# Kernel tuning notes

Hardware: AMD Instinct MI355X
Metric: run time of the kernel (lower is better)

Reference implementation:

```python
import jax, jax.numpy as jnp
import numpy as np

# ---- static dims ----
B, L, V = 8, 512, 100000
E, NERD, COREFD = 100, 20, 20          # word / ner / coref embedding dims
H, DIS, REL, HT = 128, 20, 97, 512     # hidden, dis embed, relations, n_pairs
W, N, R, C = 512, 32, 8, 256           # DNC word len, cells, read heads, ctrl hidden
IN_SIZE = E + NERD + COREFD            # 140 == H + 12 (required by final_layer)
DNC_OUT = H + 12                        # 140
CTRL_IN = IN_SIZE + R * W               # 4236
MASK_MIN, EPS, CLIP = 0.1, 1e-6, 20.0
# interface vector layout: read keys, read strengths, write key, write strength,
# erase, write vec, free gates, alloc gate, write gate, read modes,
# write mask, read masks, fwd sharpness, bwd sharpness
XI_SIZES = [R*W, R, W, 1, W, W, R, 1, 1, 3*R, W, R*W, R, R]
XI = sum(XI_SIZES)


def setup_inputs():
    key = jax.random.key(0)
    ks = iter(jax.random.split(key, 40))
    def nrm(shape, s=0.02):
        return (jax.random.normal(next(ks), shape) * s).astype(jnp.float32)
    def ri(shape, hi):
        return jax.random.randint(next(ks), shape, 0, hi)
    return dict(
        context_idxs=ri((B, L), V),
        pos=ri((B, L), L),
        context_ner=ri((B, L), 7),
        context_char_idxs=ri((B, L, 16), 262),
        context_lens=jnp.full((B,), L, dtype=jnp.int32),
        h_mapping=jax.random.uniform(next(ks), (B, HT, L), jnp.float32) / L,
        t_mapping=jax.random.uniform(next(ks), (B, HT, L), jnp.float32) / L,
        relation_mask=jnp.ones((B, HT), jnp.float32),
        dis_h_2_t=ri((B, HT), 20),
        dis_t_2_h=ri((B, HT), 20),
        word_emb=nrm((V, E), 0.1),
        entity_emb=nrm((L, COREFD), 0.1),
        ner_emb=nrm((7, NERD), 0.1),
        dis_emb=nrm((20, DIS), 0.1),
        Wih0=nrm((CTRL_IN, 4*C)), Whh0=nrm((C, 4*C)), b0=jnp.zeros((4*C,), jnp.float32),
        Wih1=nrm((C, 4*C)), Whh1=nrm((C, 4*C)), b1=jnp.zeros((4*C,), jnp.float32),
        Wih2=nrm((C, 4*C)), Whh2=nrm((C, 4*C)), b2=jnp.zeros((4*C,), jnp.float32),
        W_xi=nrm((C, XI)), b_xi=jnp.zeros((XI,), jnp.float32),
        W_out=nrm((C + R*W, DNC_OUT)), b_out=jnp.zeros((DNC_OUT,), jnp.float32),
        W_final=nrm((DNC_OUT, 2*H)), b_final=jnp.zeros((2*H,), jnp.float32),
        W_re=nrm((2*H, H)), b_re=jnp.zeros((H,), jnp.float32),
        W_bili=nrm((REL, H+DIS, H+DIS)), b_bili=jnp.zeros((REL,), jnp.float32),
    )


def _lstm(x, h, c, Wih, Whh, b):
    z = x @ Wih + h @ Whh + b
    i, f, g, o = jnp.split(z, 4, axis=-1)
    c = jax.nn.sigmoid(f) * c + jax.nn.sigmoid(i) * jnp.tanh(g)
    h = jax.nn.sigmoid(o) * jnp.tanh(c)
    return h, c


def _content(M, key_, beta, mask):
    # M [B,N,W]; key_, mask [B,h,W]; beta [B,h] -> weights [B,h,N]
    k = key_ * mask
    Mm = M[:, None] * mask[:, :, None]                 # [B,h,N,W]
    dot = jnp.einsum('bhw,bhnw->bhn', k, Mm)
    kn = jnp.linalg.norm(k, axis=-1)[..., None]
    Mn = jnp.linalg.norm(Mm, axis=-1)
    cos = dot / (kn * Mn + EPS)
    return jax.nn.softmax(beta[..., None] * cos, axis=-1)


def _sharpen(w, s):
    w = (w + EPS) ** s[..., None]
    return w / w.sum(-1, keepdims=True)


def _dnc(x, params):
    (Wih0, Whh0, b0, Wih1, Whh1, b1, Wih2, Whh2, b2, W_xi, b_xi, W_out, b_out) = params
    Bs = x.shape[0]
    eye = jnp.eye(N, dtype=x.dtype)
    splits = np.cumsum(XI_SIZES)[:-1]

    def step(carry, x_t):
        (h0, c0, h1, c1, h2, c2, M, u, wr, ww, p, Lnk, reads) = carry
        ci = jnp.concatenate([x_t, reads.reshape(Bs, R*W)], -1)
        h0, c0 = _lstm(ci, h0, c0, Wih0, Whh0, b0)
        h1, c1 = _lstm(h0, h1, c1, Wih1, Whh1, b1)
        h2, c2 = _lstm(h1, h2, c2, Wih2, Whh2, b2)
        h = jnp.clip(h2, -CLIP, CLIP)
        xi = h @ W_xi + b_xi
        (rk, rb, wk, wb, er, wv, fg, ga, gw, rm,
         wmask, rmask, sf, sb) = jnp.split(xi, splits, axis=-1)
        rk = rk.reshape(Bs, R, W)
        rb = 1 + jax.nn.softplus(rb)                    # [B,R]
        wk = wk.reshape(Bs, 1, W)
        wb = 1 + jax.nn.softplus(wb)                    # [B,1]
        er = jax.nn.sigmoid(er)                         # [B,W]
        fg = jax.nn.sigmoid(fg)                         # [B,R]
        ga = jax.nn.sigmoid(ga)
        gw = jax.nn.sigmoid(gw)
        pi = jax.nn.softmax(rm.reshape(Bs, R, 3), -1)
        wmask = MASK_MIN + (1 - MASK_MIN) * jax.nn.sigmoid(wmask)
        rmask = MASK_MIN + (1 - MASK_MIN) * jax.nn.sigmoid(rmask).reshape(Bs, R, W)
        sf = 1 + jax.nn.softplus(sf)
        sb = 1 + jax.nn.softplus(sb)

        # retention / usage
        psi = jnp.prod(1 - fg[:, :, None] * wr, axis=1)  # [B,N]
        u = (u + ww - u * ww) * psi
        # allocation weighting via sorted free list
        order = jnp.argsort(u, axis=-1)
        us = jnp.take_along_axis(u, order, -1)
        cp = jnp.cumprod(jnp.concatenate([jnp.ones((Bs, 1), u.dtype), us[:, :-1]], -1), -1)
        a_s = (1 - us) * cp
        a = jnp.zeros_like(u).at[jnp.arange(Bs)[:, None], order].set(a_s)
        # write addressing (masked content + allocation)
        cw = _content(M, wk, wb, wmask[:, None, :])[:, 0]
        ww = gw * (ga * a + (1 - ga) * cw)
        # de-allocate content of freed cells, then write
        M = M * psi[:, :, None]
        M = M * (1 - ww[:, :, None] * er[:, None, :]) + ww[:, :, None] * wv[:, None, :]
        # temporal link matrix (uses previous precedence p)
        Lnk = (1 - ww[:, :, None] - ww[:, None, :]) * Lnk + ww[:, :, None] * p[:, None, :]
        Lnk = Lnk * (1 - eye)
        p = (1 - ww.sum(-1, keepdims=True)) * p + ww
        # read addressing with link sharpness control
        fw = _sharpen(jnp.einsum('bij,brj->bri', Lnk, wr), sf)
        bw = _sharpen(jnp.einsum('bji,brj->bri', Lnk, wr), sb)
        cr = _content(M, rk, rb, rmask)
        wr = pi[..., 0:1] * bw + pi[..., 1:2] * cr + pi[..., 2:3] * fw
        reads = jnp.einsum('brn,bnw->brw', wr, M)
        y = jnp.concatenate([h, reads.reshape(Bs, R*W)], -1) @ W_out + b_out
        return (h0, c0, h1, c1, h2, c2, M, u, wr, ww, p, Lnk, reads), y

    z = jnp.zeros
    carry0 = (z((Bs, C)), z((Bs, C)), z((Bs, C)), z((Bs, C)), z((Bs, C)), z((Bs, C)),
              z((Bs, N, W)), z((Bs, N)), z((Bs, R, N)), z((Bs, N)), z((Bs, N)),
              z((Bs, N, N)), z((Bs, R, W)))
    _, ys = jax.lax.scan(step, carry0, x.transpose(1, 0, 2))
    return ys.transpose(1, 0, 2)  # [B,L,DNC_OUT]


def reference(context_idxs, pos, context_ner, context_char_idxs, context_lens,
              h_mapping, t_mapping, relation_mask, dis_h_2_t, dis_t_2_h,
              word_emb, entity_emb, ner_emb, dis_emb,
              Wih0, Whh0, b0, Wih1, Whh1, b1, Wih2, Whh2, b2,
              W_xi, b_xi, W_out, b_out, W_final, b_final, W_re, b_re,
              W_bili, b_bili):
    sent = jnp.concatenate([word_emb[context_idxs], entity_emb[pos],
                            ner_emb[context_ner]], -1)      # [B,L,140]
    dnc_params = (Wih0, Whh0, b0, Wih1, Whh1, b1, Wih2, Whh2, b2,
                  W_xi, b_xi, W_out, b_out)
    out = _dnc(sent, dnc_params)                             # [B,L,140]
    out = out @ W_final + b_final                            # LockedDropout: identity (eval)
    ctx = jax.nn.relu(out @ W_re + b_re)                     # [B,L,H]
    s0 = jnp.einsum('bpl,blh->bph', h_mapping, ctx)
    t0 = jnp.einsum('bpl,blh->bph', t_mapping, ctx)
    s_rep = jnp.concatenate([s0, dis_emb[dis_h_2_t]], -1)    # [B,P,148]
    t_rep = jnp.concatenate([t0, dis_emb[dis_t_2_h]], -1)
    return jnp.einsum('bpi,kij,bpj->bpk', s_rep, W_bili, t_rep) + b_bili
```

## Files before the change

### kernel.cpp

```cpp
#include <hip/hip_runtime.h>
#include <math.h>

#define B8      8
#define LSEQ    512
#define NWG     256
#define TPB     512
#define RELK    97
#define BI      148
#define FSTR    16
#define LDSF    39040
#define LDSB    (LDSF*4)

__device__ __forceinline__ float sigf(float x){
  return (x >= 0.f) ? 1.f/(1.f + expf(-x)) : expf(x)/(1.f + expf(x));
}
__device__ __forceinline__ float spf(float x){
  return (x > 0.f) ? x + log1pf(expf(-x)) : log1pf(expf(x));
}

__device__ __forceinline__ float agld(const float* p){
  return __hip_atomic_load(p, __ATOMIC_RELAXED, __HIP_MEMORY_SCOPE_AGENT);
}
__device__ __forceinline__ void agst(float* p, float v){
  __hip_atomic_store(p, v, __ATOMIC_RELAXED, __HIP_MEMORY_SCOPE_AGENT);
}

__global__ __launch_bounds__(256)
void k_sent(const int* __restrict__ cidx, const int* __restrict__ pos,
            const int* __restrict__ ner, const float* __restrict__ wemb,
            const float* __restrict__ eemb, const float* __restrict__ nemb,
            float* __restrict__ sent)
{
  int flat = blockIdx.x*256 + threadIdx.x;
  if (flat >= B8*LSEQ*140) return;
  int d = flat % 140; int bl = flat / 140;
  float v;
  if (d < 100)      v = wemb[(size_t)cidx[bl]*100 + d];
  else if (d < 120) v = eemb[(size_t)pos[bl]*20 + (d-100)];
  else              v = nemb[(size_t)ner[bl]*20 + (d-120)];
  sent[flat] = v;
}

__global__ __launch_bounds__(256)
void k_tr(const float* __restrict__ A, const float* __restrict__ Bsrc,
          int N, int K1a, int K1b, int K2, long long total, float* __restrict__ T)
{
  long long i = (long long)blockIdx.x*256 + threadIdx.x;
  if (i >= total) return;
  int k = (int)(i % K2);
  long long c = i / K2;
  float v = 0.f;
  if (k < K1a)            v = A[(size_t)k*N + c];
  else if (k < K1a+K1b)   v = Bsrc[(size_t)(k-K1a)*N + c];
  T[i] = v;
}

__device__ __forceinline__ void gbar(int* flags, int* genrep, int seq){
  __syncthreads();
  const int tid = threadIdx.x;
  const int bid = blockIdx.x;
  if (tid == 0){
    asm volatile("s_waitcnt vmcnt(0)" ::: "memory");
    __hip_atomic_store(&flags[bid*FSTR], seq, __ATOMIC_RELAXED, __HIP_MEMORY_SCOPE_AGENT);
  }
  if (bid == 0){
    if (tid < NWG){
      while (__hip_atomic_load(&flags[tid*FSTR], __ATOMIC_RELAXED, __HIP_MEMORY_SCOPE_AGENT) < seq)
        __builtin_amdgcn_s_sleep(2);
    }
    __syncthreads();
    if (tid < 32)
      __hip_atomic_store(&genrep[tid*FSTR], seq, __ATOMIC_RELAXED, __HIP_MEMORY_SCOPE_AGENT);
  } else if (tid == 0){
    while (__hip_atomic_load(&genrep[(bid & 31)*FSTR], __ATOMIC_RELAXED, __HIP_MEMORY_SCOPE_AGENT) < seq)
      __builtin_amdgcn_s_sleep(2);
  }
  __syncthreads();
}

__device__ void mem_phase(float* lds, const float* __restrict__ xi,
                          float* __restrict__ M, float* u_g, float* ww_g,
                          float* p_g, float* wr_g, float* L_g, float* rout)
{
  const int tid = threadIdx.x;
  float* mL  = lds;
  float* mwr = lds+1024;
  float* mwrn= lds+1280;
  float* mcr = lds+1536;
  float* mfw = lds+1792;
  float* mbw = lds+2048;
  float* PSI = lds+2304;
  float* UU  = lds+2336;
  float* US  = lds+2368;
  float* AA  = lds+2400;
  float* CW  = lds+2432;
  float* WWN = lds+2464;
  float* WWO = lds+2496;
  float* PP  = lds+2528;
  int*   mord= (int*)(lds+2560);
  float* mh  = lds+2592;
  float* mpi = lds+2656;
  float* msc = lds+2688;
  float* q1  = lds+2752;
  float* q2  = lds+3264;

  if (tid < 8){
    mh[tid]    = 1.f + spf(agld(&xi[4096+tid]));
    mh[8+tid]  = 1.f + spf(agld(&xi[10283+tid]));
    mh[16+tid] = 1.f + spf(agld(&xi[10291+tid]));
    mh[24+tid] = sigf(agld(&xi[5641+tid]));
    float e0=agld(&xi[5651+3*tid]), e1=agld(&xi[5652+3*tid]), e2=agld(&xi[5653+3*tid]);
    float mx=fmaxf(e0,fmaxf(e1,e2));
    float x0=expf(e0-mx), x1=expf(e1-mx), x2=expf(e2-mx);
    float inv=1.f/(x0+x1+x2);
    mpi[tid*3]=x0*inv; mpi[tid*3+1]=x1*inv; mpi[tid*3+2]=x2*inv;
  }
  if (tid==0){ msc[0]=1.f+spf(agld(&xi[4616])); msc[1]=sigf(agld(&xi[5649])); msc[2]=sigf(agld(&xi[5650])); }
  if (tid<32){ UU[tid]=u_g[tid]; WWO[tid]=ww_g[tid]; PP[tid]=p_g[tid]; }
  if (tid<256) mwr[tid]=wr_g[tid];
  mL[tid]=L_g[tid]; mL[tid+512]=L_g[tid+512];
  { float wm = 0.1f+0.9f*sigf(agld(&xi[5675+tid])); q1[tid]=agld(&xi[4104+tid])*wm; q2[tid]=wm; }
  __syncthreads();

  if (tid<32){
    float psi=1.f;
    #pragma unroll
    for (int r=0;r<8;r++) psi *= (1.f - mh[24+r]*mwr[r*32+tid]);
    PSI[tid]=psi;
    float uo=UU[tid], wo=WWO[tid];
    UU[tid]=(uo+wo-uo*wo)*psi;
  }
  __syncthreads();
  if (tid<32){
    float un=UU[tid]; int rank=0;
    for (int m=0;m<32;m++){ float um=UU[m]; rank += (um<un)||(um==un && m<tid); }
    mord[rank]=tid;
  }
  __syncthreads();
  if (tid<32) US[tid]=UU[mord[tid]];
  __syncthreads();
  if (tid==0){ float cp=1.f; for (int j=0;j<32;j++){ AA[mord[j]]=(1.f-US[j])*cp; cp*=US[j]; } }
  __syncthreads();

  { float q=q1[tid]*q1[tid];
    for (int o=32;o;o>>=1) q += __shfl_down(q,o,64);
    if ((tid&63)==0) msc[8+(tid>>6)]=q; }
  __syncthreads();
  if (tid==0){ float q=0.f; for (int i=0;i<8;i++) q+=msc[8+i]; msc[3]=sqrtf(q); }
  __syncthreads();
  { int n=tid>>4, wsub=tid&15;
    float d=0.f,q=0.f;
    for (int i=0;i<32;i++){ int w=wsub+16*i; float m=M[(size_t)n*512+w]; float t2=m*q2[w]; d+=q1[w]*t2; q+=t2*t2; }
    for (int o=8;o;o>>=1){ d+=__shfl_down(d,o,16); q+=__shfl_down(q,o,16); }
    if (wsub==0){ float cs=d/(msc[3]*sqrtf(q)+1e-6f); CW[n]=msc[0]*cs; } }
  __syncthreads();
  if (tid==0){ float mx=-1e30f; for(int n=0;n<32;n++) mx=fmaxf(mx,CW[n]); msc[4]=mx; }
  __syncthreads();
  if (tid<32) CW[tid]=expf(CW[tid]-msc[4]);
  __syncthreads();
  if (tid==0){ float sm=0.f; for(int n=0;n<32;n++) sm+=CW[n]; msc[5]=1.f/sm; }
  __syncthreads();
  if (tid<32) CW[tid]*=msc[5];
  __syncthreads();
  if (tid<32) WWN[tid]=msc[2]*(msc[1]*AA[tid]+(1.f-msc[1])*CW[tid]);
  __syncthreads();
  { float er=sigf(agld(&xi[4617+tid])); float wv=agld(&xi[5129+tid]);
    for (int n=0;n<32;n++){ size_t idx=(size_t)n*512+tid; float m=M[idx];
      M[idx]=m*PSI[n]*(1.f-WWN[n]*er)+WWN[n]*wv; } }
  __syncthreads();
  for (int ii=0;ii<2;ii++){ int f=tid+512*ii; int i=f>>5, j=f&31;
    float nl=(1.f-WWN[i]-WWN[j])*mL[f]+WWN[i]*PP[j];
    mL[f]=(i==j)?0.f:nl; }
  __syncthreads();
  if (tid==0){ float sw=0.f; for(int n=0;n<32;n++) sw+=WWN[n]; msc[6]=sw; }
  __syncthreads();
  if (tid<32) PP[tid]=(1.f-msc[6])*PP[tid]+WWN[tid];
  __syncthreads();
  { int r=(tid>>5)&7, i=tid&31; bool isB=(tid>=256);
    float accv=0.f;
    if (!isB){ for (int j=0;j<32;j++) accv += mL[i*32+j]*mwr[r*32+j]; }
    else     { for (int j=0;j<32;j++) accv += mL[j*32+i]*mwr[r*32+j]; }
    float sp = isB? mh[16+r] : mh[8+r];
    float e = expf(sp*logf(accv+1e-6f));
    if (!isB) mfw[r*32+i]=e; else mbw[r*32+i]=e; }
  __syncthreads();
  if (tid<16){ int r=tid&7; float sm=0.f;
    if (tid<8){ for(int n=0;n<32;n++) sm+=mfw[r*32+n]; msc[16+r]=1.f/sm; }
    else      { for(int n=0;n<32;n++) sm+=mbw[r*32+n]; msc[24+r]=1.f/sm; } }
  __syncthreads();
  { int r=(tid>>5)&7, i=tid&31; bool isB=(tid>=256);
    if (!isB) mfw[r*32+i]*=msc[16+r]; else mbw[r*32+i]*=msc[24+r]; }
  __syncthreads();
  for (int r=0;r<8;r++){
    { float rm=0.1f+0.9f*sigf(agld(&xi[6187+r*512+tid]));
      q1[tid]=agld(&xi[r*512+tid])*rm; q2[tid]=rm; }
    __syncthreads();
    { float q=q1[tid]*q1[tid];
      for (int o=32;o;o>>=1) q+=__shfl_down(q,o,64);
      if ((tid&63)==0) msc[8+(tid>>6)]=q; }
    __syncthreads();
    if (tid==0){ float qq=0.f; for(int i=0;i<8;i++) qq+=msc[8+i]; msc[32]=sqrtf(qq); }
    __syncthreads();
    { int n=tid>>4, wsub=tid&15;
      float d=0.f,q=0.f;
      for (int i=0;i<32;i++){ int w=wsub+16*i; float m=M[(size_t)n*512+w]; float t2=m*q2[w]; d+=q1[w]*t2; q+=t2*t2; }
      for (int o=8;o;o>>=1){ d+=__shfl_down(d,o,16); q+=__shfl_down(q,o,16); }
      if (wsub==0){ float cs=d/(msc[32]*sqrtf(q)+1e-6f); mcr[r*32+n]=mh[r]*cs; } }
    __syncthreads();
  }
  if (tid<8){ int r=tid; float mx=-1e30f;
    for (int n=0;n<32;n++) mx=fmaxf(mx,mcr[r*32+n]);
    float sm=0.f;
    for (int n=0;n<32;n++){ float e=expf(mcr[r*32+n]-mx); mcr[r*32+n]=e; sm+=e; }
    float inv=1.f/sm;
    for (int n=0;n<32;n++) mcr[r*32+n]*=inv; }
  __syncthreads();
  if (tid<256){ int r=tid>>5, n=tid&31;
    float v=mpi[r*3]*mbw[r*32+n]+mpi[r*3+1]*mcr[r*32+n]+mpi[r*3+2]*mfw[r*32+n];
    mwrn[tid]=v; wr_g[tid]=v; }
  __syncthreads();
  { int r=tid>>6, wsub=tid&63;
    for (int i2=0;i2<8;i2++){ int w=wsub+64*i2;
      float accv=0.f;
      for (int n=0;n<32;n++) accv+=mwrn[r*32+n]*M[(size_t)n*512+w];
      agst(&rout[r*512+w], accv); } }
  if (tid<32){ u_g[tid]=UU[tid]; ww_g[tid]=WWN[tid]; p_g[tid]=PP[tid]; }
  L_g[tid]=mL[tid]; L_g[tid+512]=mL[tid+512];
}

__global__ __launch_bounds__(TPB, 1)
void dnc_persist(
  const float* __restrict__ sent,
  const float* __restrict__ WAg, const float* __restrict__ b0,
  const float* __restrict__ W1g, const float* __restrict__ b1,
  const float* __restrict__ W2g, const float* __restrict__ b2,
  const float* __restrict__ WXIg,const float* __restrict__ bxi,
  const float* __restrict__ WY,  const float* __restrict__ bout,
  float* __restrict__ Hh, float* __restrict__ yh,
  float* __restrict__ reads2,
  float* __restrict__ h0g, float* __restrict__ h1g, float* __restrict__ h2g,
  float* __restrict__ c0g, float* __restrict__ c1g, float* __restrict__ c2g,
  float* __restrict__ z0g, float* __restrict__ z1g, float* __restrict__ z2g,
  float* __restrict__ xig,
  float* __restrict__ Mb, float* __restrict__ ug, float* __restrict__ wwg,
  float* __restrict__ pg, float* __restrict__ wrg, float* __restrict__ Lg,
  int* flags, int* genrep)
{
  extern __shared__ float lds[];
  float* sA   = lds;
  float* sRed = lds + 4160;
  float* wA   = lds + 4224;
  float* w1l  = lds + 22656;
  float* w2l  = lds + 24704;
  float* wxl  = lds + 26752;
  const int wg  = blockIdx.x;
  const int tid = threadIdx.x;
  const int cq = tid >> 7, kq = tid & 127;
  const int xc = tid >> 6, xk = tid & 63;
  int seq = 0;

  for (int f=tid; f<18432; f+=TPB) wA[f]  = WAg[(size_t)wg*18432 + f];
  for (int f=tid; f<2048;  f+=TPB) w1l[f] = W1g[(size_t)wg*2048  + f];
  for (int f=tid; f<2048;  f+=TPB) w2l[f] = W2g[(size_t)wg*2048  + f];
  for (int f=tid; f<12288; f+=TPB){
    int cl = f>>8, k = f&255; int col = wg*48 + cl;
    wxl[f] = (col < 10299) ? WXIg[(size_t)col*256 + k] : 0.f;
  }
  const bool isy = (wg >= 8 && wg < 148);
  const float* wcolY = WY + (size_t)(isy ? (wg-8) : 0)*4352;
  __syncthreads();

  #pragma unroll 1
  for (int t=0; t<LSEQ; t++){
    const int rp = t&1, wp = rp^1, pprev = (t+1)&1;
    const float* readsPrev = reads2 + (size_t)pprev*32768;

    {
      const float* h0p = h0g + pprev*2048;
      float acc[8] = {0,0,0,0,0,0,0,0};
      float av[8];
      #pragma unroll
      for (int s=0;s<8;s++){
        int kg = tid;
        av[s] = (kg<140) ? sent[((size_t)s*512 + t)*140 + kg]
                         : agld(&readsPrev[s*4096 + kg - 140]);
      }
      #pragma unroll 1
      for (int ch=0; ch<9; ch++){
        __syncthreads();
        #pragma unroll
        for (int s=0;s<8;s++) sA[s*520 + tid] = av[s];
        __syncthreads();
        if (ch < 8){
          int kg = (ch+1)*512 + tid;
          #pragma unroll
          for (int s=0;s<8;s++){
            float v;
            if (kg < 140)       v = sent[((size_t)s*512 + t)*140 + kg];
            else if (kg < 4236) v = agld(&readsPrev[s*4096 + kg - 140]);
            else if (kg < 4492) v = agld(&h0p[s*256 + (kg-4236)]);
            else                v = 0.f;
            av[s]=v;
          }
        }
        float4 wv = *reinterpret_cast<const float4*>(&wA[cq*4608 + ch*512 + (kq<<2)]);
        #pragma unroll
        for (int s=0;s<8;s++){
          float4 a = *reinterpret_cast<const float4*>(&sA[s*520 + (kq<<2)]);
          acc[s] += a.x*wv.x + a.y*wv.y + a.z*wv.z + a.w*wv.w;
        }
      }
      #pragma unroll
      for (int o=32;o;o>>=1)
        #pragma unroll
        for (int s=0;s<8;s++) acc[s]+=__shfl_down(acc[s],o,64);
      if ((tid&63)==0){ int wv2=tid>>6;
        #pragma unroll
        for (int s=0;s<8;s++) sRed[wv2*8+s]=acc[s]; }
      __syncthreads();
      if (tid<32){ int c=tid>>3, s=tid&7;
        agst(&z0g[s*1024 + wg*4 + c], sRed[c*16+s] + sRed[c*16+8+s] + b0[wg*4+c]); }
    }
    gbar(flags,genrep,++seq);

    {
      float4 w1v = *reinterpret_cast<const float4*>(&w1l[cq*512 + (kq<<2)]);
      if (tid<256){
        int j=tid;
        #pragma unroll
        for (int s=0;s<8;s++){
          float zi=agld(&z0g[s*1024+j]), zf=agld(&z0g[s*1024+256+j]);
          float zg=agld(&z0g[s*1024+512+j]), zo=agld(&z0g[s*1024+768+j]);
          float cold=agld(&c0g[rp*2048+s*256+j]);
          float cn=sigf(zf)*cold+sigf(zi)*tanhf(zg);
          float h=sigf(zo)*tanhf(cn);
          sA[s*520+j]=h;
          if (wg==8){ agst(&c0g[wp*2048+s*256+j],cn); agst(&h0g[rp*2048+s*256+j],h); }
        }
      } else {
        int j=tid-256;
        const float* h1p = h1g + pprev*2048;
        #pragma unroll
        for (int s=0;s<8;s++) sA[s*520+256+j]=agld(&h1p[s*256+j]);
      }
      __syncthreads();
      float acc[8]={0,0,0,0,0,0,0,0};
      #pragma unroll
      for (int s=0;s<8;s++){
        float4 a=*reinterpret_cast<const float4*>(&sA[s*520+(kq<<2)]);
        acc[s]+=a.x*w1v.x+a.y*w1v.y+a.z*w1v.z+a.w*w1v.w;
      }
      #pragma unroll
      for (int o=32;o;o>>=1)
        #pragma unroll
        for (int s=0;s<8;s++) acc[s]+=__shfl_down(acc[s],o,64);
      if ((tid&63)==0){ int wv2=tid>>6;
        #pragma unroll
        for (int s=0;s<8;s++) sRed[wv2*8+s]=acc[s]; }
      __syncthreads();
      if (tid<32){ int c=tid>>3, s=tid&7;
        agst(&z1g[s*1024 + wg*4 + c], sRed[c*16+s] + sRed[c*16+8+s] + b1[wg*4+c]); }
    }
    gbar(flags,genrep,++seq);

    {
      float4 w2v = *reinterpret_cast<const float4*>(&w2l[cq*512 + (kq<<2)]);
      if (tid<256){
        int j=tid;
        #pragma unroll
        for (int s=0;s<8;s++){
          float zi=agld(&z1g[s*1024+j]), zf=agld(&z1g[s*1024+256+j]);
          float zg=agld(&z1g[s*1024+512+j]), zo=agld(&z1g[s*1024+768+j]);
          float cold=agld(&c1g[rp*2048+s*256+j]);
          float cn=sigf(zf)*cold+sigf(zi)*tanhf(zg);
          float h=sigf(zo)*tanhf(cn);
          sA[s*520+j]=h;
          if (wg==8){ agst(&c1g[wp*2048+s*256+j],cn); agst(&h1g[rp*2048+s*256+j],h); }
        }
      } else {
        int j=tid-256;
        const float* h2p = h2g + pprev*2048;
        #pragma unroll
        for (int s=0;s<8;s++) sA[s*520+256+j]=agld(&h2p[s*256+j]);
      }
      __syncthreads();
      float acc[8]={0,0,0,0,0,0,0,0};
      #pragma unroll
      for (int s=0;s<8;s++){
        float4 a=*reinterpret_cast<const float4*>(&sA[s*520+(kq<<2)]);
        acc[s]+=a.x*w2v.x+a.y*w2v.y+a.z*w2v.z+a.w*w2v.w;
      }
      #pragma unroll
      for (int o=32;o;o>>=1)
        #pragma unroll
        for (int s=0;s<8;s++) acc[s]+=__shfl_down(acc[s],o,64);
      if ((tid&63)==0){ int wv2=tid>>6;
        #pragma unroll
        for (int s=0;s<8;s++) sRed[wv2*8+s]=acc[s]; }
      __syncthreads();
      if (tid<32){ int c=tid>>3, s=tid&7;
        agst(&z2g[s*1024 + wg*4 + c], sRed[c*16+s] + sRed[c*16+8+s] + b2[wg*4+c]); }
    }
    gbar(flags,genrep,++seq);

    {
      if (tid<256){
        int j=tid;
        #pragma unroll
        for (int s=0;s<8;s++){
          float zi=agld(&z2g[s*1024+j]), zf=agld(&z2g[s*1024+256+j]);
          float zg=agld(&z2g[s*1024+512+j]), zo=agld(&z2g[s*1024+768+j]);
          float cold=agld(&c2g[rp*2048+s*256+j]);
          float cn=sigf(zf)*cold+sigf(zi)*tanhf(zg);
          float h2=sigf(zo)*tanhf(cn);
          float hc=fminf(fmaxf(h2,-20.f),20.f);
          sA[s*520+j]=hc;
          if (wg==8){ agst(&c2g[wp*2048+s*256+j],cn); agst(&h2g[rp*2048+s*256+j],h2);
                      agst(&Hh[((size_t)t*8+s)*256+j],hc); }
        }
      }
      __syncthreads();
      float accx[6][8];
      #pragma unroll
      for (int cc=0;cc<6;cc++)
        #pragma unroll
        for (int s=0;s<8;s++) accx[cc][s]=0.f;
      #pragma unroll
      for (int s=0;s<8;s++){
        float4 a = *reinterpret_cast<const float4*>(&sA[s*520 + (xk<<2)]);
        #pragma unroll
        for (int cc=0;cc<6;cc++){
          float4 wv = *reinterpret_cast<const float4*>(&wxl[(xc*6+cc)*256 + (xk<<2)]);
          accx[cc][s] += a.x*wv.x + a.y*wv.y + a.z*wv.z + a.w*wv.w;
        }
      }
      #pragma unroll
      for (int o=32;o;o>>=1)
        #pragma unroll
        for (int cc=0;cc<6;cc++)
          #pragma unroll
          for (int s=0;s<8;s++) accx[cc][s]+=__shfl_down(accx[cc][s],o,64);
      if ((tid&63)==0){
        #pragma unroll
        for (int cc=0;cc<6;cc++){
          int col = wg*48 + xc*6 + cc;
          if (col < 10299){
            #pragma unroll
            for (int s=0;s<8;s++) agst(&xig[(size_t)s*10299+col], accx[cc][s]+bxi[col]);
          }
        }
      }
    }
    gbar(flags,genrep,++seq);

    if (wg < 8){
      mem_phase(lds, xig + (size_t)wg*10299, Mb + (size_t)wg*16384,
                ug+wg*32, wwg+wg*32, pg+wg*32, wrg+wg*256, Lg+wg*1024,
                reads2 + (size_t)rp*32768 + wg*4096);
    } else if (isy && t > 0){
      int ty = t-1;
      const float* rdp = reads2 + (size_t)(ty&1)*32768;
      float wy[9];
      #pragma unroll
      for (int ch=0;ch<9;ch++){ int k=ch*512+tid; wy[ch]=(k<4352)? wcolY[k] : 0.f; }
      float acy[8]={0,0,0,0,0,0,0,0};
      #pragma unroll
      for (int ch=0;ch<9;ch++){
        int kg=ch*512+tid;
        #pragma unroll
        for (int s=0;s<8;s++){
          float a;
          if (kg<256)       a=agld(&Hh[((size_t)ty*8+s)*256+kg]);
          else if (kg<4352) a=agld(&rdp[s*4096+kg-256]);
          else              a=0.f;
          acy[s]+=a*wy[ch];
        }
      }
      #pragma unroll
      for (int o=32;o;o>>=1)
        #pragma unroll
        for (int s=0;s<8;s++) acy[s]+=__shfl_down(acy[s],o,64);
      if ((tid&63)==0){ int wv2=tid>>6;
        #pragma unroll
        for (int s=0;s<8;s++) sRed[wv2*8+s]=acy[s]; }
      __syncthreads();
      if (tid<8){ float v=0.f;
        #pragma unroll
        for (int w=0;w<8;w++) v+=sRed[w*8+tid];
        yh[((size_t)tid*512+ty)*140+(wg-8)]=v+bout[wg-8]; }
    }
    gbar(flags,genrep,++seq);
  }

  if (isy){
    int ty = 511;
    const float* rdp = reads2 + (size_t)(ty&1)*32768;
    float wy[9];
    #pragma unroll
    for (int ch=0;ch<9;ch++){ int k=ch*512+tid; wy[ch]=(k<4352)? wcolY[k] : 0.f; }
    float acy[8]={0,0,0,0,0,0,0,0};
    #pragma unroll
    for (int ch=0;ch<9;ch++){
      int kg=ch*512+tid;
      #pragma unroll
      for (int s=0;s<8;s++){
        float a;
        if (kg<256)       a=agld(&Hh[((size_t)ty*8+s)*256+kg]);
        else if (kg<4352) a=agld(&rdp[s*4096+kg-256]);
        else              a=0.f;
        acy[s]+=a*wy[ch];
      }
    }
    #pragma unroll
    for (int o=32;o;o>>=1)
      #pragma unroll
      for (int s=0;s<8;s++) acy[s]+=__shfl_down(acy[s],o,64);
    if ((tid&63)==0){ int wv2=tid>>6;
      #pragma unroll
      for (int s=0;s<8;s++) sRed[wv2*8+s]=acy[s]; }
    __syncthreads();
    if (tid<8){ float v=0.f;
      #pragma unroll
      for (int w=0;w<8;w++) v+=sRed[w*8+tid];
      yh[((size_t)tid*512+ty)*140+(wg-8)]=v+bout[wg-8]; }
  }
}

__global__ __launch_bounds__(256)
void gemm16(int M, int N, int K,
            const float* __restrict__ A, long long sAb, int lda,
            const float* __restrict__ Bm, long long sBb, int ldb,
            float* __restrict__ C, long long sCb, int ldc,
            const float* __restrict__ bias, int relu)
{
  __shared__ float sAh[16*512];
  const int tid = threadIdx.x;
  const float* Ab = A + (size_t)blockIdx.y*sAb;
  const float* Bb = Bm + (size_t)blockIdx.y*sBb;
  float* Cb = C + (size_t)blockIdx.y*sCb;
  const int m0 = blockIdx.x*16;
  const int tot = 16*K;
  for (int f = tid; f < tot; f += 256) sAh[f] = Ab[(size_t)m0*lda + f];
  __syncthreads();
  int c = (tid & 63)*4; int rg = tid >> 6;
  if (c >= N) return;
  float acc[4][4] = {};
  for (int k=0;k<K;k++){
    float4 bv = *reinterpret_cast<const float4*>(Bb + (size_t)k*ldb + c);
    #pragma unroll
    for (int rr=0;rr<4;rr++){
      float a = sAh[(rg*4+rr)*K + k];
      acc[rr][0] += a*bv.x; acc[rr][1] += a*bv.y; acc[rr][2] += a*bv.z; acc[rr][3] += a*bv.w;
    }
  }
  for (int rr=0;rr<4;rr++){
    int m = m0 + rg*4 + rr;
    #pragma unroll
    for (int e=0;e<4;e++){
      float v = acc[rr][e] + (bias ? bias[c+e] : 0.f);
      if (relu) v = fmaxf(v, 0.f);
      Cb[(size_t)m*ldc + c + e] = v;
    }
  }
}

__global__ __launch_bounds__(256)
void bilin(const float* __restrict__ s0, const float* __restrict__ t0,
           const float* __restrict__ dis_emb, const int* __restrict__ dht,
           const int* __restrict__ dth, const float* __restrict__ Wb,
           const float* __restrict__ bb, float* __restrict__ out)
{
  __shared__ float sS[BI][33];
  __shared__ float sT[32][152];
  const int tid = threadIdx.x;
  const int bp0 = blockIdx.x*32;
  for (int f = tid; f < 32*BI; f += 256){
    int pp = f / BI, i = f % BI;
    int bp = bp0 + pp;
    float sv, tv;
    if (i < 128){ sv = s0[(size_t)bp*128 + i]; tv = t0[(size_t)bp*128 + i]; }
    else {
      sv = dis_emb[(size_t)dht[bp]*20 + (i-128)];
      tv = dis_emb[(size_t)dth[bp]*20 + (i-128)];
    }
    sS[i][pp] = sv; sT[pp][i] = tv;
  }
  __syncthreads();
  const int ppg = tid >> 5, jb = tid & 31;
  const int pp0 = ppg*4;
  const int k0 = blockIdx.y*49, kend = min(k0+49, RELK);
  for (int k = k0; k < kend; k++){
    const float* Wk = Wb + (size_t)k*BI*BI;
    float acc[4][5];
    #pragma unroll
    for (int a=0;a<4;a++) for (int b=0;b<5;b++) acc[a][b]=0.f;
    for (int i=0;i<BI;i++){
      float sv0 = sS[i][pp0], sv1 = sS[i][pp0+1], sv2 = sS[i][pp0+2], sv3 = sS[i][pp0+3];
      const float* wrow = Wk + i*BI;
      #pragma unroll
      for (int jj=0;jj<5;jj++){
        int j = jb + 32*jj;
        if (j < BI){
          float w = wrow[j];
          acc[0][jj] += sv0*w; acc[1][jj] += sv1*w; acc[2][jj] += sv2*w; acc[3][jj] += sv3*w;
        }
      }
    }
    float dot[4] = {0.f,0.f,0.f,0.f};
    #pragma unroll
    for (int jj=0;jj<5;jj++){
      int j = jb + 32*jj;
      if (j < BI){
        #pragma unroll
        for (int p4=0;p4<4;p4++) dot[p4] += acc[p4][jj]*sT[pp0+p4][j];
      }
    }
    #pragma unroll
    for (int p4=0;p4<4;p4++)
      for (int o=16;o;o>>=1) dot[p4] += __shfl_down(dot[p4], o, 32);
    if (jb == 0){
      #pragma unroll
      for (int p4=0;p4<4;p4++)
        out[(size_t)(bp0+pp0+p4)*RELK + k] = dot[p4] + bb[k];
    }
  }
}

extern "C" void kernel_launch(void* const* d_in, const int* in_sizes, int n_in,
                              void* d_out, int out_size, void* d_ws, size_t ws_size,
                              hipStream_t stream)
{
  (void)in_sizes; (void)n_in; (void)out_size; (void)ws_size;
  const int*   ctx_idx = (const int*)  d_in[0];
  const int*   pos     = (const int*)  d_in[1];
  const int*   nerI    = (const int*)  d_in[2];
  const float* h_map   = (const float*)d_in[5];
  const float* t_map   = (const float*)d_in[6];
  const int*   dht     = (const int*)  d_in[8];
  const int*   dth     = (const int*)  d_in[9];
  const float* wemb    = (const float*)d_in[10];
  const float* eemb    = (const float*)d_in[11];
  const float* nemb    = (const float*)d_in[12];
  const float* demb    = (const float*)d_in[13];
  const float* Wih0    = (const float*)d_in[14];
  const float* Whh0    = (const float*)d_in[15];
  const float* b0      = (const float*)d_in[16];
  const float* Wih1    = (const float*)d_in[17];
  const float* Whh1    = (const float*)d_in[18];
  const float* b1      = (const float*)d_in[19];
  const float* Wih2    = (const float*)d_in[20];
  const float* Whh2    = (const float*)d_in[21];
  const float* b2      = (const float*)d_in[22];
  const float* Wxi     = (const float*)d_in[23];
  const float* bxi     = (const float*)d_in[24];
  const float* Wout    = (const float*)d_in[25];
  const float* bout    = (const float*)d_in[26];
  const float* Wfin    = (const float*)d_in[27];
  const float* bfin    = (const float*)d_in[28];
  const float* Wre     = (const float*)d_in[29];
  const float* bre     = (const float*)d_in[30];
  const float* Wbili   = (const float*)d_in[31];
  const float* bbili   = (const float*)d_in[32];

  float* ws    = (float*)d_ws;
  float* sent  = ws;
  float* Hh    = sent + 573440;
  float* yh    = Hh + 1048576;
  float* s0b   = yh + 573440;
  float* t0b   = s0b + 524288;
  float* reads2= t0b + 524288;
  float* h0g   = reads2 + 65536;
  float* h1g   = h0g + 4096;
  float* h2g   = h1g + 4096;
  float* c0g   = h2g + 4096;
  float* c1g   = c0g + 4096;
  float* c2g   = c1g + 4096;
  float* z0g   = c2g + 4096;
  float* z1g   = z0g + 8192;
  float* z2g   = z1g + 8192;
  float* xig   = z2g + 8192;
  float* Mb    = xig + 82392;
  float* ug    = Mb + 131072;
  float* wwg   = ug + 256;
  float* pg    = wwg + 256;
  float* wrg   = pg + 256;
  float* Lg    = wrg + 2048;
  float* barf  = Lg + 8192;
  float* WA_T  = barf + 4608;
  float* W1T   = WA_T + 4718592;
  float* W2T   = W1T + 524288;
  float* WXIT  = W2T + 524288;
  float* WYT   = WXIT + 2636544;
  float* o256  = Hh;
  float* ctxb  = sent;
  int* flags  = (int*)barf;
  int* genrep = flags + 256*FSTR;

  size_t stateFloats = (size_t)(WA_T - reads2);
  hipMemsetAsync(reads2, 0, stateFloats*sizeof(float), stream);

  hipLaunchKernelGGL(k_tr, dim3(18432), dim3(256), 0, stream,
                     Wih0, Whh0, 1024, 4236, 256, 4608, (long long)4718592, WA_T);
  hipLaunchKernelGGL(k_tr, dim3(2048), dim3(256), 0, stream,
                     Wih1, Whh1, 1024, 256, 256, 512, (long long)524288, W1T);
  hipLaunchKernelGGL(k_tr, dim3(2048), dim3(256), 0, stream,
                     Wih2, Whh2, 1024, 256, 256, 512, (long long)524288, W2T);
  hipLaunchKernelGGL(k_tr, dim3(10299), dim3(256), 0, stream,
                     Wxi, Wxi, 10299, 256, 0, 256, (long long)2636544, WXIT);
  hipLaunchKernelGGL(k_tr, dim3(2380), dim3(256), 0, stream,
                     Wout, Wout, 140, 4352, 0, 4352, (long long)609280, WYT);

  hipLaunchKernelGGL(k_sent, dim3((573440+255)/256), dim3(256), 0, stream,
                     ctx_idx, pos, nerI, wemb, eemb, nemb, sent);

  hipFuncSetAttribute(reinterpret_cast<const void*>(dnc_persist),
                      hipFuncAttributeMaxDynamicSharedMemorySize, LDSB);

  hipLaunchKernelGGL(dnc_persist, dim3(NWG), dim3(TPB), LDSB, stream,
                     sent, WA_T, b0, W1T, b1, W2T, b2, WXIT, bxi, WYT, bout,
                     Hh, yh, reads2,
                     h0g, h1g, h2g, c0g, c1g, c2g, z0g, z1g, z2g, xig,
                     Mb, ug, wwg, pg, wrg, Lg, flags, genrep);

  hipLaunchKernelGGL(gemm16, dim3(256,1), dim3(256), 0, stream,
                     4096, 256, 140, yh, (long long)0, 140, Wfin, (long long)0, 256,
                     o256, (long long)0, 256, bfin, 0);
  hipLaunchKernelGGL(gemm16, dim3(256,1), dim3(256), 0, stream,
                     4096, 128, 256, o256, (long long)0, 256, Wre, (long long)0, 128,
                     ctxb, (long long)0, 128, bre, 1);
  hipLaunchKernelGGL(gemm16, dim3(32,8), dim3(256), 0, stream,
                     512, 128, 512, h_map, (long long)(512*512), 512,
                     ctxb, (long long)(512*128), 128,
                     s0b, (long long)(512*128), 128, (const float*)nullptr, 0);
  hipLaunchKernelGGL(gemm16, dim3(32,8), dim3(256), 0, stream,
                     512, 128, 512, t_map, (long long)(512*512), 512,
                     ctxb, (long long)(512*128), 128,
                     t0b, (long long)(512*128), 128, (const float*)nullptr, 0);
  hipLaunchKernelGGL(bilin, dim3(128,2), dim3(256), 0, stream,
                     s0b, t0b, demb, dht, dth, Wbili, bbili, (float*)d_out);
}
```

Before: 88.91 ms.

## Replicate shared recurrent state into per-group copies and stagger global reads

Producers of the DNC recurrent state (gate pre-activations, hidden and cell states, read vectors, clipped controller output) now write NC=8 copies. Each group of 32 workgroups reads its own copy, and workgroups start from a rotated chunk or index, so that many workgroups do not hit the same L2 lines at once. The grid barrier now gives each workgroup its own release flag and polls with a shorter sleep. The cost is 8x more atomic stores per step and a larger workspace, and the extra stores sit on the critical path between barriers.

```diff
diff --git a/kernel.cpp b/kernel.cpp
--- a/kernel.cpp
+++ b/kernel.cpp
@@ -10,6 +10,8 @@
 #define FSTR    16
 #define LDSF    39040
 #define LDSB    (LDSF*4)
+#define NC      8
+#define RCPY    32768
 
 __device__ __forceinline__ float sigf(float x){
   return (x >= 0.f) ? 1.f/(1.f + expf(-x)) : expf(x)/(1.f + expf(x));
@@ -66,21 +68,21 @@
   if (bid == 0){
     if (tid < NWG){
       while (__hip_atomic_load(&flags[tid*FSTR], __ATOMIC_RELAXED, __HIP_MEMORY_SCOPE_AGENT) < seq)
-        __builtin_amdgcn_s_sleep(2);
+        __builtin_amdgcn_s_sleep(1);
     }
     __syncthreads();
-    if (tid < 32)
+    if (tid < NWG)
       __hip_atomic_store(&genrep[tid*FSTR], seq, __ATOMIC_RELAXED, __HIP_MEMORY_SCOPE_AGENT);
   } else if (tid == 0){
-    while (__hip_atomic_load(&genrep[(bid & 31)*FSTR], __ATOMIC_RELAXED, __HIP_MEMORY_SCOPE_AGENT) < seq)
-      __builtin_amdgcn_s_sleep(2);
+    while (__hip_atomic_load(&genrep[bid*FSTR], __ATOMIC_RELAXED, __HIP_MEMORY_SCOPE_AGENT) < seq)
+      __builtin_amdgcn_s_sleep(1);
   }
   __syncthreads();
 }
 
 __device__ void mem_phase(float* lds, const float* __restrict__ xi,
                           float* __restrict__ M, float* u_g, float* ww_g,
-                          float* p_g, float* wr_g, float* L_g, float* rout)
+                          float* p_g, float* wr_g, float* L_g, float* rout0)
 {
   const int tid = threadIdx.x;
   float* mL  = lds;
@@ -223,7 +225,8 @@
     for (int i2=0;i2<8;i2++){ int w=wsub+64*i2;
       float accv=0.f;
       for (int n=0;n<32;n++) accv+=mwrn[r*32+n]*M[(size_t)n*512+w];
-      agst(&rout[r*512+w], accv); } }
+      #pragma unroll
+      for (int c2=0;c2<NC;c2++) agst(&rout0[(size_t)c2*RCPY + r*512+w], accv); } }
   if (tid<32){ u_g[tid]=UU[tid]; ww_g[tid]=WWN[tid]; p_g[tid]=PP[tid]; }
   L_g[tid]=mL[tid]; L_g[tid+512]=mL[tid+512];
 }
@@ -236,7 +239,7 @@
   const float* __restrict__ W2g, const float* __restrict__ b2,
   const float* __restrict__ WXIg,const float* __restrict__ bxi,
   const float* __restrict__ WY,  const float* __restrict__ bout,
-  float* __restrict__ Hh, float* __restrict__ yh,
+  float* __restrict__ Hh, float* __restrict__ yh, float* __restrict__ Hy,
   float* __restrict__ reads2,
   float* __restrict__ h0g, float* __restrict__ h1g, float* __restrict__ h2g,
   float* __restrict__ c0g, float* __restrict__ c1g, float* __restrict__ c2g,
@@ -257,6 +260,10 @@
   const int tid = threadIdx.x;
   const int cq = tid >> 7, kq = tid & 127;
   const int xc = tid >> 6, xk = tid & 63;
+  const int cp = wg >> 5;
+  const int kk = (tid + (wg<<4)) & 511;
+  const int jj = (tid + (wg<<4)) & 255;
+  const int ptid = kk;
   int seq = 0;
 
   for (int f=tid; f<18432; f+=TPB) wA[f]  = WAg[(size_t)wg*18432 + f];
@@ -267,32 +274,45 @@
     wxl[f] = (col < 10299) ? WXIg[(size_t)col*256 + k] : 0.f;
   }
   const bool isy = (wg >= 8 && wg < 148);
+  const bool iscw = (wg >= 8 && wg < 16);
+  const int  gcw = wg - 8;
   const float* wcolY = WY + (size_t)(isy ? (wg-8) : 0)*4352;
   __syncthreads();
 
   #pragma unroll 1
   for (int t=0; t<LSEQ; t++){
     const int rp = t&1, wp = rp^1, pprev = (t+1)&1;
-    const float* readsPrev = reads2 + (size_t)pprev*32768;
+    const float* readsPrev = reads2 + ((size_t)pprev*NC + cp)*RCPY;
+    const float* h0p = h0g + ((size_t)pprev*NC + cp)*2048;
+    const float* h1p = h1g + ((size_t)pprev*NC + cp)*2048;
+    const float* h2p = h2g + ((size_t)pprev*NC + cp)*2048;
 
     {
-      const float* h0p = h0g + pprev*2048;
       float acc[8] = {0,0,0,0,0,0,0,0};
       float av[8];
-      #pragma unroll
-      for (int s=0;s<8;s++){
-        int kg = tid;
-        av[s] = (kg<140) ? sent[((size_t)s*512 + t)*140 + kg]
-                         : agld(&readsPrev[s*4096 + kg - 140]);
+      int ch = wg % 9;
+      {
+        int kg = ch*512 + kk;
+        #pragma unroll
+        for (int s=0;s<8;s++){
+          float v;
+          if (kg < 140)       v = sent[((size_t)s*512 + t)*140 + kg];
+          else if (kg < 4236) v = agld(&readsPrev[s*4096 + kg - 140]);
+          else if (kg < 4492) v = agld(&h0p[s*256 + (kg-4236)]);
+          else                v = 0.f;
+          av[s]=v;
+        }
       }
       #pragma unroll 1
-      for (int ch=0; ch<9; ch++){
+      for (int ci=0; ci<9; ci++){
         __syncthreads();
         #pragma unroll
-        for (int s=0;s<8;s++) sA[s*520 + tid] = av[s];
+        for (int s=0;s<8;s++) sA[s*520 + kk] = av[s];
         __syncthreads();
-        if (ch < 8){
-          int kg = (ch+1)*512 + tid;
+        const int cur = ch;
+        ch = (ch+1 == 9) ? 0 : ch+1;
+        if (ci < 8){
+          int kg = ch*512 + kk;
           #pragma unroll
           for (int s=0;s<8;s++){
             float v;
@@ -303,7 +323,7 @@
             av[s]=v;
           }
         }
-        float4 wv = *reinterpret_cast<const float4*>(&wA[cq*4608 + ch*512 + (kq<<2)]);
+        float4 wv = *reinterpret_cast<const float4*>(&wA[cq*4608 + cur*512 + (kq<<2)]);
         #pragma unroll
         for (int s=0;s<8;s++){
           float4 a = *reinterpret_cast<const float4*>(&sA[s*520 + (kq<<2)]);
@@ -319,29 +339,31 @@
         for (int s=0;s<8;s++) sRed[wv2*8+s]=acc[s]; }
       __syncthreads();
       if (tid<32){ int c=tid>>3, s=tid&7;
-        agst(&z0g[s*1024 + wg*4 + c], sRed[c*16+s] + sRed[c*16+8+s] + b0[wg*4+c]); }
+        float v = sRed[c*16+s] + sRed[c*16+8+s] + b0[wg*4+c];
+        #pragma unroll
+        for (int c2=0;c2<NC;c2++) agst(&z0g[(size_t)c2*8192 + s*1024 + wg*4 + c], v); }
     }
     gbar(flags,genrep,++seq);
 
     {
+      const float* z0c = z0g + (size_t)cp*8192;
       float4 w1v = *reinterpret_cast<const float4*>(&w1l[cq*512 + (kq<<2)]);
       if (tid<256){
-        int j=tid;
         #pragma unroll
         for (int s=0;s<8;s++){
-          float zi=agld(&z0g[s*1024+j]), zf=agld(&z0g[s*1024+256+j]);
-          float zg=agld(&z0g[s*1024+512+j]), zo=agld(&z0g[s*1024+768+j]);
-          float cold=agld(&c0g[rp*2048+s*256+j]);
+          float zi=agld(&z0c[s*1024+jj]), zf=agld(&z0c[s*1024+256+jj]);
+          float zg=agld(&z0c[s*1024+512+jj]), zo=agld(&z0c[s*1024+768+jj]);
+          float cold=agld(&c0g[((size_t)rp*NC+cp)*2048+s*256+jj]);
           float cn=sigf(zf)*cold+sigf(zi)*tanhf(zg);
           float h=sigf(zo)*tanhf(cn);
-          sA[s*520+j]=h;
-          if (wg==8){ agst(&c0g[wp*2048+s*256+j],cn); agst(&h0g[rp*2048+s*256+j],h); }
+          sA[s*520+jj]=h;
+          if (iscw){ agst(&c0g[((size_t)wp*NC+gcw)*2048+s*256+jj],cn);
+                     agst(&h0g[((size_t)rp*NC+gcw)*2048+s*256+jj],h); }
         }
       } else {
-        int j=tid-256;
-        const float* h1p = h1g + pprev*2048;
-        #pragma unroll
-        for (int s=0;s<8;s++) sA[s*520+256+j]=agld(&h1p[s*256+j]);
+        int j2=(tid-256 + (wg<<4)) & 255;
+        #pragma unroll
+        for (int s=0;s<8;s++) sA[s*520+256+j2]=agld(&h1p[s*256+j2]);
       }
       __syncthreads();
       float acc[8]={0,0,0,0,0,0,0,0};
@@ -359,29 +381,31 @@
         for (int s=0;s<8;s++) sRed[wv2*8+s]=acc[s]; }
       __syncthreads();
       if (tid<32){ int c=tid>>3, s=tid&7;
-        agst(&z1g[s*1024 + wg*4 + c], sRed[c*16+s] + sRed[c*16+8+s] + b1[wg*4+c]); }
+        float v = sRed[c*16+s] + sRed[c*16+8+s] + b1[wg*4+c];
+        #pragma unroll
+        for (int c2=0;c2<NC;c2++) agst(&z1g[(size_t)c2*8192 + s*1024 + wg*4 + c], v); }
     }
     gbar(flags,genrep,++seq);
 
     {
+      const float* z1c = z1g + (size_t)cp*8192;
       float4 w2v = *reinterpret_cast<const float4*>(&w2l[cq*512 + (kq<<2)]);
       if (tid<256){
-        int j=tid;
         #pragma unroll
         for (int s=0;s<8;s++){
-          float zi=agld(&z1g[s*1024+j]), zf=agld(&z1g[s*1024+256+j]);
-          float zg=agld(&z1g[s*1024+512+j]), zo=agld(&z1g[s*1024+768+j]);
-          float cold=agld(&c1g[rp*2048+s*256+j]);
+          float zi=agld(&z1c[s*1024+jj]), zf=agld(&z1c[s*1024+256+jj]);
+          float zg=agld(&z1c[s*1024+512+jj]), zo=agld(&z1c[s*1024+768+jj]);
+          float cold=agld(&c1g[((size_t)rp*NC+cp)*2048+s*256+jj]);
           float cn=sigf(zf)*cold+sigf(zi)*tanhf(zg);
           float h=sigf(zo)*tanhf(cn);
-          sA[s*520+j]=h;
-          if (wg==8){ agst(&c1g[wp*2048+s*256+j],cn); agst(&h1g[rp*2048+s*256+j],h); }
+          sA[s*520+jj]=h;
+          if (iscw){ agst(&c1g[((size_t)wp*NC+gcw)*2048+s*256+jj],cn);
+                     agst(&h1g[((size_t)rp*NC+gcw)*2048+s*256+jj],h); }
         }
       } else {
-        int j=tid-256;
-        const float* h2p = h2g + pprev*2048;
-        #pragma unroll
-        for (int s=0;s<8;s++) sA[s*520+256+j]=agld(&h2p[s*256+j]);
+        int j2=(tid-256 + (wg<<4)) & 255;
+        #pragma unroll
+        for (int s=0;s<8;s++) sA[s*520+256+j2]=agld(&h2p[s*256+j2]);
       }
       __syncthreads();
       float acc[8]={0,0,0,0,0,0,0,0};
@@ -399,24 +423,28 @@
         for (int s=0;s<8;s++) sRed[wv2*8+s]=acc[s]; }
       __syncthreads();
       if (tid<32){ int c=tid>>3, s=tid&7;
-        agst(&z2g[s*1024 + wg*4 + c], sRed[c*16+s] + sRed[c*16+8+s] + b2[wg*4+c]); }
+        float v = sRed[c*16+s] + sRed[c*16+8+s] + b2[wg*4+c];
+        #pragma unroll
+        for (int c2=0;c2<NC;c2++) agst(&z2g[(size_t)c2*8192 + s*1024 + wg*4 + c], v); }
     }
     gbar(flags,genrep,++seq);
 
     {
+      const float* z2c = z2g + (size_t)cp*8192;
       if (tid<256){
-        int j=tid;
         #pragma unroll
         for (int s=0;s<8;s++){
-          float zi=agld(&z2g[s*1024+j]), zf=agld(&z2g[s*1024+256+j]);
-          float zg=agld(&z2g[s*1024+512+j]), zo=agld(&z2g[s*1024+768+j]);
-          float cold=agld(&c2g[rp*2048+s*256+j]);
+          float zi=agld(&z2c[s*1024+jj]), zf=agld(&z2c[s*1024+256+jj]);
+          float zg=agld(&z2c[s*1024+512+jj]), zo=agld(&z2c[s*1024+768+jj]);
+          float cold=agld(&c2g[((size_t)rp*NC+cp)*2048+s*256+jj]);
           float cn=sigf(zf)*cold+sigf(zi)*tanhf(zg);
           float h2=sigf(zo)*tanhf(cn);
           float hc=fminf(fmaxf(h2,-20.f),20.f);
-          sA[s*520+j]=hc;
-          if (wg==8){ agst(&c2g[wp*2048+s*256+j],cn); agst(&h2g[rp*2048+s*256+j],h2);
-                      agst(&Hh[((size_t)t*8+s)*256+j],hc); }
+          sA[s*520+jj]=hc;
+          if (iscw){ agst(&c2g[((size_t)wp*NC+gcw)*2048+s*256+jj],cn);
+                     agst(&h2g[((size_t)rp*NC+gcw)*2048+s*256+jj],h2);
+                     agst(&Hy[((size_t)rp*NC+gcw)*2048+s*256+jj],hc);
+                     if (wg==8) Hh[((size_t)t*8+s)*256+jj]=hc; }
         }
       }
       __syncthreads();
@@ -456,21 +484,23 @@
     if (wg < 8){
       mem_phase(lds, xig + (size_t)wg*10299, Mb + (size_t)wg*16384,
                 ug+wg*32, wwg+wg*32, pg+wg*32, wrg+wg*256, Lg+wg*1024,
-                reads2 + (size_t)rp*32768 + wg*4096);
+                reads2 + (size_t)rp*NC*RCPY + wg*4096);
     } else if (isy && t > 0){
       int ty = t-1;
-      const float* rdp = reads2 + (size_t)(ty&1)*32768;
+      const float* rdp = reads2 + ((size_t)(ty&1)*NC + cp)*RCPY;
+      const float* Hyp = Hy + ((size_t)(ty&1)*NC + cp)*2048;
       float wy[9];
       #pragma unroll
-      for (int ch=0;ch<9;ch++){ int k=ch*512+tid; wy[ch]=(k<4352)? wcolY[k] : 0.f; }
+      for (int ch=0;ch<9;ch++){ int k=ch*512+ptid; wy[ch]=(k<4352)? wcolY[k] : 0.f; }
       float acy[8]={0,0,0,0,0,0,0,0};
       #pragma unroll
-      for (int ch=0;ch<9;ch++){
-        int kg=ch*512+tid;
+      for (int ci=0;ci<9;ci++){
+        int ch = (ci + wg) % 9;
+        int kg = ch*512+ptid;
         #pragma unroll
         for (int s=0;s<8;s++){
           float a;
-          if (kg<256)       a=agld(&Hh[((size_t)ty*8+s)*256+kg]);
+          if (kg<256)       a=agld(&Hyp[s*256+kg]);
           else if (kg<4352) a=agld(&rdp[s*4096+kg-256]);
           else              a=0.f;
           acy[s]+=a*wy[ch];
@@ -494,18 +524,20 @@
 
   if (isy){
     int ty = 511;
-    const float* rdp = reads2 + (size_t)(ty&1)*32768;
+    const float* rdp = reads2 + ((size_t)(ty&1)*NC + cp)*RCPY;
+    const float* Hyp = Hy + ((size_t)(ty&1)*NC + cp)*2048;
     float wy[9];
     #pragma unroll
-    for (int ch=0;ch<9;ch++){ int k=ch*512+tid; wy[ch]=(k<4352)? wcolY[k] : 0.f; }
+    for (int ch=0;ch<9;ch++){ int k=ch*512+ptid; wy[ch]=(k<4352)? wcolY[k] : 0.f; }
     float acy[8]={0,0,0,0,0,0,0,0};
     #pragma unroll
-    for (int ch=0;ch<9;ch++){
-      int kg=ch*512+tid;
+    for (int ci=0;ci<9;ci++){
+      int ch = (ci + wg) % 9;
+      int kg = ch*512+ptid;
       #pragma unroll
       for (int s=0;s<8;s++){
         float a;
-        if (kg<256)       a=agld(&Hh[((size_t)ty*8+s)*256+kg]);
+        if (kg<256)       a=agld(&Hyp[s*256+kg]);
         else if (kg<4352) a=agld(&rdp[s*4096+kg-256]);
         else              a=0.f;
         acy[s]+=a*wy[ch];
@@ -669,16 +701,17 @@
   float* s0b   = yh + 573440;
   float* t0b   = s0b + 524288;
   float* reads2= t0b + 524288;
-  float* h0g   = reads2 + 65536;
-  float* h1g   = h0g + 4096;
-  float* h2g   = h1g + 4096;
-  float* c0g   = h2g + 4096;
-  float* c1g   = c0g + 4096;
-  float* c2g   = c1g + 4096;
-  float* z0g   = c2g + 4096;
-  float* z1g   = z0g + 8192;
-  float* z2g   = z1g + 8192;
-  float* xig   = z2g + 8192;
+  float* h0g   = reads2 + 524288;
+  float* h1g   = h0g + 32768;
+  float* h2g   = h1g + 32768;
+  float* c0g   = h2g + 32768;
+  float* c1g   = c0g + 32768;
+  float* c2g   = c1g + 32768;
+  float* z0g   = c2g + 32768;
+  float* z1g   = z0g + 65536;
+  float* z2g   = z1g + 65536;
+  float* Hy    = z2g + 65536;
+  float* xig   = Hy + 32768;
   float* Mb    = xig + 82392;
   float* ug    = Mb + 131072;
   float* wwg   = ug + 256;
@@ -686,7 +719,7 @@
   float* wrg   = pg + 256;
   float* Lg    = wrg + 2048;
   float* barf  = Lg + 8192;
-  float* WA_T  = barf + 4608;
+  float* WA_T  = barf + 8192;
   float* W1T   = WA_T + 4718592;
   float* W2T   = W1T + 524288;
   float* WXIT  = W2T + 524288;
@@ -718,7 +751,7 @@
 
   hipLaunchKernelGGL(dnc_persist, dim3(NWG), dim3(TPB), LDSB, stream,
                      sent, WA_T, b0, W1T, b1, W2T, b2, WXIT, bxi, WYT, bout,
-                     Hh, yh, reads2,
+                     Hh, yh, Hy, reads2,
                      h0g, h1g, h2g, c0g, c1g, c2g, z0g, z1g, z2g, xig,
                      Mb, ug, wwg, pg, wrg, Lg, flags, genrep);
 
```

New measurement: 97.40 ms. 9.5% more time.
